# Kernel optimization log

Hardware: AMD Instinct MI355X
Metric: run time of the kernel (lower is better)

The kernel has to match this reference:

```python
import jax, jax.numpy as jnp
import numpy as np

N, E, G, D = 100000, 1600000, 1000, 32
EPS = 1e-5


def setup_inputs() -> dict:
    key = jax.random.key(0)
    ks = jax.random.split(key, 24)
    inp = {
        'h': jax.random.normal(ks[0], (N, D), dtype=jnp.float32),
        'src': jax.random.randint(ks[1], (E,), 0, N, dtype=jnp.int32),
        'dst': jax.random.randint(ks[2], (E,), 0, N, dtype=jnp.int32),
        'graph_id': jnp.sort(jax.random.randint(ks[3], (N,), 0, G, dtype=jnp.int32)),
    }
    dims = [D, 32, 32, 32, 1]
    ki = 4
    for i in range(4):
        inp[f'conv_w{i}'] = jax.random.normal(ks[ki], (dims[i], dims[i + 1]), dtype=jnp.float32) * 0.1; ki += 1
        inp[f'conv_b{i}'] = jax.random.normal(ks[ki], (dims[i + 1],), dtype=jnp.float32) * 0.1; ki += 1
        inp[f'bn_g{i}'] = jnp.ones((dims[i + 1],), dtype=jnp.float32)
        inp[f'bn_b{i}'] = jnp.zeros((dims[i + 1],), dtype=jnp.float32)
    mlp_dims = [D + 32 + 32 + 32 + 1, 128, 64, 1]  # 129 -> 128 -> 64 -> 1
    for i in range(3):
        inp[f'mlp_w{i}'] = jax.random.normal(ks[ki], (mlp_dims[i], mlp_dims[i + 1]), dtype=jnp.float32) * 0.1; ki += 1
        inp[f'mlp_b{i}'] = jax.random.normal(ks[ki], (mlp_dims[i + 1],), dtype=jnp.float32) * 0.1; ki += 1
    return inp


def _mean_agg(x, src, dst):
    # DGL update_all(copy_u, mean): h'_v = mean of h_u over in-neighbors u of v
    deg = jax.ops.segment_sum(jnp.ones((src.shape[0],), x.dtype), dst, num_segments=N)
    agg = jax.ops.segment_sum(x[src], dst, num_segments=N)
    return agg / jnp.maximum(deg, 1.0)[:, None]


def _bn(x, g, b):
    # BatchNorm1d in training mode: batch statistics over node dim
    m = x.mean(axis=0)
    v = x.var(axis=0)
    return g * (x - m) * jax.lax.rsqrt(v + EPS) + b


def reference(h, src, dst, graph_id,
              conv_w0, conv_b0, conv_w1, conv_b1, conv_w2, conv_b2, conv_w3, conv_b3,
              bn_g0, bn_b0, bn_g1, bn_b1, bn_g2, bn_b2, bn_g3, bn_b3,
              mlp_w0, mlp_b0, mlp_w1, mlp_b1, mlp_w2, mlp_b2):
    conv = [(conv_w0, conv_b0), (conv_w1, conv_b1), (conv_w2, conv_b2), (conv_w3, conv_b3)]
    bn = [(bn_g0, bn_b0), (bn_g1, bn_b1), (bn_g2, bn_b2), (bn_g3, bn_b3)]
    h_list = [h]
    x = h
    for (w, b), (g, bb) in zip(conv, bn):
        x = _mean_agg(x, src, dst) @ w + b      # GCNConv
        x = jax.nn.relu(_bn(x, g, bb))           # BN + ReLU
        h_list.append(x)
    h_final = jnp.concatenate(h_list, axis=1)    # [N, 129]
    # dgl.mean_nodes: per-graph mean pool
    cnt = jax.ops.segment_sum(jnp.ones((N,), h_final.dtype), graph_id, num_segments=G)
    hg = jax.ops.segment_sum(h_final, graph_id, num_segments=G) / jnp.maximum(cnt, 1.0)[:, None]
    hg = jax.nn.relu(hg @ mlp_w0 + mlp_b0)
    hg = jax.nn.relu(hg @ mlp_w1 + mlp_b1)
    hg = hg @ mlp_w2 + mlp_b2
    return hg.reshape(-1)                         # [G]
```

## Files before the change

### kernel.cpp

```cpp
#include <hip/hip_runtime.h>

#define NSLOT 32
#define BN_EPS 1e-5f
#define NSB 256
#define BKBITS 8
#define BKN 256
#define MAXBUCK 512

static inline int cdiv_h(int a, int b) { return (a + b - 1) / b; }

__device__ __forceinline__ float4 f4add(float4 a, float4 b) {
    return make_float4(a.x + b.x, a.y + b.y, a.z + b.z, a.w + b.w);
}

__device__ __forceinline__ unsigned bf16rtn(float x) {
    unsigned u = __float_as_uint(x);
    return (u + 0x7FFFu + ((u >> 16) & 1u)) >> 16;
}
__device__ __forceinline__ unsigned bf16pack2(float lo, float hi) {
    return bf16rtn(lo) | (bf16rtn(hi) << 16);
}

__device__ __forceinline__ int blk_excl_scan256(int v, int t) {
    __shared__ int wsum[4];
    int l = t & 63, w = t >> 6;
    int incl = v;
#pragma unroll
    for (int off = 1; off < 64; off <<= 1) {
        int o = __shfl_up(incl, off, 64);
        if (l >= off) incl += o;
    }
    if (l == 63) wsum[w] = incl;
    __syncthreads();
    int wofs = 0;
#pragma unroll
    for (int i = 0; i < 4; i++) wofs += (i < w) ? wsum[i] : 0;
    __syncthreads();
    return wofs + incl - v;
}

__device__ __forceinline__ int blk_excl_scan512(int v, int t) {
    __shared__ int wsum8[8];
    int l = t & 63, w = t >> 6;
    int incl = v;
#pragma unroll
    for (int off = 1; off < 64; off <<= 1) {
        int o = __shfl_up(incl, off, 64);
        if (l >= off) incl += o;
    }
    if (l == 63) wsum8[w] = incl;
    __syncthreads();
    int wofs = 0;
#pragma unroll
    for (int i = 0; i < 8; i++) wofs += (i < w) ? wsum8[i] : 0;
    __syncthreads();
    return wofs + incl - v;
}

__device__ __forceinline__ void bn_coef(const float* __restrict__ sSum, const float* __restrict__ sSq,
                                        const float* __restrict__ bg, const float* __restrict__ bb,
                                        float invN, int ch, float* aOut, float* cOut) {
    float S = 0.f, Q = 0.f;
#pragma unroll
    for (int s = 0; s < NSLOT; s++) { S += sSum[s * 32 + ch]; Q += sSq[s * 32 + ch]; }
    float m = S * invN;
    float var = Q * invN - m * m;
    if (var < 0.f) var = 0.f;
    float iv = rsqrtf(var + BN_EPS);
    float a = bg[ch] * iv;
    *aOut = a;
    *cOut = bb[ch] - m * a;
}


__global__ __launch_bounds__(256) void k_hist(const int* __restrict__ dst, int* __restrict__ histT,
                                              float* __restrict__ sSum, float* __restrict__ sSq,
                                              int E, int nbuck, int chunk) {
    __shared__ int bins[MAXBUCK];
    int k = blockIdx.x, t = threadIdx.x;
    if (k == 0) {
        for (int i = t; i < 4 * NSLOT * 32; i += 256) { sSum[i] = 0.f; sSq[i] = 0.f; }
    }
    for (int b = t; b < nbuck; b += 256) bins[b] = 0;
    __syncthreads();
    int lo = k * chunk, hi = lo + chunk; if (hi > E) hi = E;
    for (int i = lo + t; i < hi; i += 256) atomicAdd(&bins[dst[i] >> BKBITS], 1);
    __syncthreads();
    for (int b = t; b < nbuck; b += 256) histT[k * nbuck + b] = bins[b];
}


__global__ __launch_bounds__(256) void k_scanA(const int* __restrict__ histT, int* __restrict__ prefixB,
                                               int* __restrict__ totalP, int* __restrict__ totalU,
                                               const int* __restrict__ gid, int* __restrict__ gstart,
                                               int nbuck, int N, int G) {
    int b = blockIdx.x, k = threadIdx.x;
    int i = b * 256 + k;
    if (i < N) {
        int g = gid[i];
        int gp = (i == 0) ? -1 : gid[i - 1];
        for (int x = gp + 1; x <= g; ++x) gstart[x] = i;
        if (i == N - 1) { for (int x = g + 1; x <= G; ++x) gstart[x] = N; }
    }
    int c = histT[k * nbuck + b];
    int pad = (c + 15) & ~15;
    int ep = blk_excl_scan256(pad, k);
    prefixB[b * NSB + k] = ep;
    int ec = blk_excl_scan256(c, k);
    if (k == NSB - 1) { totalP[b] = ep + pad; totalU[b] = ec + c; }
}

__global__ __launch_bounds__(512) void k_scanB(const int* __restrict__ totalP, const int* __restrict__ totalU,
                                               int* __restrict__ baseP, int* __restrict__ baseU, int nbuck) {
    int t = threadIdx.x;
    int vp = (t < nbuck) ? totalP[t] : 0;
    int vu = (t < nbuck) ? totalU[t] : 0;
    int ep = blk_excl_scan512(vp, t);
    int eu = blk_excl_scan512(vu, t);
    if (t < nbuck) { baseP[t] = ep; baseU[t] = eu; }
}


__global__ __launch_bounds__(256) void k_scatter2(const int* __restrict__ src, const int* __restrict__ dst,
                                                  const int* __restrict__ baseP, const int* __restrict__ prefixB,
                                                  unsigned* __restrict__ ebuf, int E, int nbuck, int chunk) {
    __shared__ int cur[MAXBUCK];
    int k = blockIdx.x, t = threadIdx.x;
    for (int b = t; b < nbuck; b += 256) cur[b] = baseP[b] + prefixB[b * NSB + k];
    __syncthreads();
    int lo = k * chunk, hi = lo + chunk; if (hi > E) hi = E;
    for (int i = lo + t; i < hi; i += 256) {
        int d = dst[i], s = src[i];
        int b = d >> BKBITS;
        int pos = atomicAdd(&cur[b], 1);
        ebuf[pos] = ((unsigned)(d & (BKN - 1)) << 24) | (unsigned)s;
    }
}


__global__ __launch_bounds__(256) void k_sortb(const unsigned* __restrict__ ebuf, const int* __restrict__ histT,
                                               const int* __restrict__ baseP, const int* __restrict__ prefixB,
                                               const int* __restrict__ baseU,
                                               int* __restrict__ col, int* __restrict__ rs, int* __restrict__ re,
                                               int nbuck, int N) {
    __shared__ int binCnt[BKN], binStart[BKN], cursor[BKN];
    __shared__ int cellBase[NSB], cellCnt[NSB];
    int b = blockIdx.x, t = threadIdx.x;
    cellBase[t] = baseP[b] + prefixB[b * NSB + t];
    cellCnt[t]  = histT[t * nbuck + b];
    binCnt[t] = 0; cursor[t] = 0;
    __syncthreads();
    {
        int cb = cellBase[t], cc = cellCnt[t];
        for (int j = 0; j < cc; j++) atomicAdd(&binCnt[ebuf[cb + j] >> 24], 1);
    }
    __syncthreads();
    int bs = blk_excl_scan256(binCnt[t], t);
    binStart[t] = bs;
    __syncthreads();
    int colBase = baseU[b];
    {
        int cb = cellBase[t], cc = cellCnt[t];
        for (int j = 0; j < cc; j++) {
            unsigned e = ebuf[cb + j];
            int l = e >> 24;
            int pos = binStart[l] + atomicAdd(&cursor[l], 1);
            col[colBase + pos] = (int)(e & 0xFFFFFFu);
        }
    }
    int node = b * BKN + t;
    if (node < N) {
        rs[node] = colBase + binStart[t];
        re[node] = colBase + binStart[t] + binCnt[t];
    }
}


template <int AFF>
__global__ __launch_bounds__(256) void k_transform(const float* __restrict__ xin, const float* __restrict__ W,
                                                   const float* __restrict__ sSum, const float* __restrict__ sSq,
                                                   const float* __restrict__ bg, const float* __restrict__ bb,
                                                   uint4* __restrict__ pb, int n, float invN) {
    __shared__ float sW[32][32];
    __shared__ float sA[32], sC[32];
    int t = threadIdx.x;
    for (int i = t; i < 1024; i += 256) sW[i >> 5][i & 31] = W[i];
    if (AFF && t < 32) bn_coef(sSum, sSq, bg, bb, invN, t, &sA[t], &sC[t]);
    __syncthreads();
    int node = blockIdx.x * 256 + t;
    if (node >= n) return;
    float x[32];
    const float4* s4 = (const float4*)(xin + (size_t)node * 32);
#pragma unroll
    for (int q = 0; q < 8; q++) {
        float4 v = s4[q];
        x[4*q] = v.x; x[4*q+1] = v.y; x[4*q+2] = v.z; x[4*q+3] = v.w;
    }
    if (AFF) {
#pragma unroll
        for (int k = 0; k < 32; k++) {
            float v = sA[k] * x[k] + sC[k];
            x[k] = v > 0.f ? v : 0.f;
        }
    }
    float acc[32];
#pragma unroll
    for (int f = 0; f < 32; f++) acc[f] = 0.f;
#pragma unroll
    for (int k = 0; k < 32; k++) {
        float xv = x[k];
#pragma unroll
        for (int f = 0; f < 32; f++) acc[f] += xv * sW[k][f];
    }
    uint4* d4 = pb + (size_t)node * 4;
#pragma unroll
    for (int q = 0; q < 4; q++) {
        uint4 o;
        o.x = bf16pack2(acc[8*q+0], acc[8*q+1]);
        o.y = bf16pack2(acc[8*q+2], acc[8*q+3]);
        o.z = bf16pack2(acc[8*q+4], acc[8*q+5]);
        o.w = bf16pack2(acc[8*q+6], acc[8*q+7]);
        d4[q] = o;
    }
}

__global__ __launch_bounds__(256) void k_transform3(const float* __restrict__ y2, const float* __restrict__ w3,
                                                    const float* __restrict__ sSum, const float* __restrict__ sSq,
                                                    const float* __restrict__ bg, const float* __restrict__ bb,
                                                    float* __restrict__ p3, int n, float invN) {
    __shared__ float sw[32], sA[32], sC[32];
    int t = threadIdx.x;
    if (t < 32) { sw[t] = w3[t]; bn_coef(sSum, sSq, bg, bb, invN, t, &sA[t], &sC[t]); }
    __syncthreads();
    int i = blockIdx.x * 256 + t;
    if (i >= n) return;
    const float4* x4 = (const float4*)(y2 + (size_t)i * 32);
    float acc = 0.f;
#pragma unroll
    for (int q = 0; q < 8; q++) {
        float4 v = x4[q];
        float vv[4] = {v.x, v.y, v.z, v.w};
#pragma unroll
        for (int r = 0; r < 4; r++) {
            int k = q * 4 + r;
            float xv = sA[k] * vv[r] + sC[k];
            xv = xv > 0.f ? xv : 0.f;
            acc += xv * sw[k];
        }
    }
    p3[i] = acc;
}


__global__ __launch_bounds__(256) void k_aggregate(const uint4* __restrict__ pb, const int* __restrict__ rs,
                                                   const int* __restrict__ re, const int* __restrict__ col,
                                                   const float* __restrict__ bias,
                                                   float4* __restrict__ y4, float* __restrict__ sSum,
                                                   float* __restrict__ sSq, int n) {
    __shared__ int scol[2048];
    int t = threadIdx.x;
    int lane = t & 3;
    int grp = t >> 2;
    int node0 = blockIdx.x * 64;
    int node = node0 + grp;
    int base0 = 0, len = 0;
    if (node0 < n) {
        int last = node0 + 63; if (last > n - 1) last = n - 1;
        base0 = rs[node0];
        len = re[last] - base0;
    }
    bool lds = (len > 0 && len <= 2048);
    if (lds) { for (int i = t; i < len; i += 256) scol[i] = col[base0 + i]; }
    __syncthreads();

    float accA[8], accB[8];
#pragma unroll
    for (int q = 0; q < 8; q++) { accA[q] = 0.f; accB[q] = 0.f; }
    float vout[8];
#pragma unroll
    for (int q = 0; q < 8; q++) vout[q] = 0.f;
    if (node < n) {
        int s0 = rs[node], s1 = re[node];
#define GATH(vv, c) uint4 vv = pb[(size_t)(c) * 4 + lane]
#define ACC(dst, vv) \
        dst[0] += __uint_as_float((vv).x << 16); dst[1] += __uint_as_float((vv).x & 0xFFFF0000u); \
        dst[2] += __uint_as_float((vv).y << 16); dst[3] += __uint_as_float((vv).y & 0xFFFF0000u); \
        dst[4] += __uint_as_float((vv).z << 16); dst[5] += __uint_as_float((vv).z & 0xFFFF0000u); \
        dst[6] += __uint_as_float((vv).w << 16); dst[7] += __uint_as_float((vv).w & 0xFFFF0000u)
        if (lds) {
            int j = s0 - base0, j1 = s1 - base0;
            for (; j + 8 <= j1; j += 8) {
                int c0 = scol[j], c1 = scol[j + 1], c2 = scol[j + 2], c3 = scol[j + 3];
                int c4 = scol[j + 4], c5 = scol[j + 5], c6 = scol[j + 6], c7 = scol[j + 7];
                GATH(g0, c0); GATH(g1, c1); GATH(g2, c2); GATH(g3, c3);
                GATH(g4, c4); GATH(g5, c5); GATH(g6, c6); GATH(g7, c7);
                ACC(accA, g0); ACC(accB, g1); ACC(accA, g2); ACC(accB, g3);
                ACC(accA, g4); ACC(accB, g5); ACC(accA, g6); ACC(accB, g7);
            }
            for (; j < j1; ++j) { GATH(g, scol[j]); ACC(accA, g); }
        } else {
            for (int j = s0; j < s1; ++j) { GATH(g, col[j]); ACC(accA, g); }
        }
#undef GATH
#undef ACC
        int deg = s1 - s0;
        float inv = (deg > 0) ? 1.f / (float)deg : 1.f;
        const float4* b4 = (const float4*)bias;
        float4 b0 = b4[lane * 2], b1 = b4[lane * 2 + 1];
        vout[0] = (accA[0] + accB[0]) * inv + b0.x;
        vout[1] = (accA[1] + accB[1]) * inv + b0.y;
        vout[2] = (accA[2] + accB[2]) * inv + b0.z;
        vout[3] = (accA[3] + accB[3]) * inv + b0.w;
        vout[4] = (accA[4] + accB[4]) * inv + b1.x;
        vout[5] = (accA[5] + accB[5]) * inv + b1.y;
        vout[6] = (accA[6] + accB[6]) * inv + b1.z;
        vout[7] = (accA[7] + accB[7]) * inv + b1.w;
        y4[(size_t)node * 8 + lane * 2]     = make_float4(vout[0], vout[1], vout[2], vout[3]);
        y4[(size_t)node * 8 + lane * 2 + 1] = make_float4(vout[4], vout[5], vout[6], vout[7]);
    }
    __shared__ float sS[64][32];
    __shared__ float sQ[64][32];
    ((float4*)&sS[grp][lane * 8])[0] = make_float4(vout[0], vout[1], vout[2], vout[3]);
    ((float4*)&sS[grp][lane * 8])[1] = make_float4(vout[4], vout[5], vout[6], vout[7]);
    ((float4*)&sQ[grp][lane * 8])[0] = make_float4(vout[0]*vout[0], vout[1]*vout[1], vout[2]*vout[2], vout[3]*vout[3]);
    ((float4*)&sQ[grp][lane * 8])[1] = make_float4(vout[4]*vout[4], vout[5]*vout[5], vout[6]*vout[6], vout[7]*vout[7]);
    __syncthreads();
    if (t < 32) {
        float S = 0.f, Q = 0.f;
#pragma unroll
        for (int g2 = 0; g2 < 64; g2++) { S += sS[g2][t]; Q += sQ[g2][t]; }
        int slot = blockIdx.x & (NSLOT - 1);
        atomicAdd(&sSum[slot * 32 + t], S);
        atomicAdd(&sSq[slot * 32 + t], Q);
    }
}

__global__ __launch_bounds__(256) void k_aggregate3(const float* __restrict__ p3, const int* __restrict__ rs,
                                                    const int* __restrict__ re, const int* __restrict__ col,
                                                    const float* __restrict__ b1,
                                                    float* __restrict__ y3, float* __restrict__ sSum,
                                                    float* __restrict__ sSq, int n) {
    int i = blockIdx.x * 256 + threadIdx.x;
    float lsum = 0.f, lsq = 0.f;
    if (i < n) {
        int s0 = rs[i], s1 = re[i];
        float a0 = 0.f, a1 = 0.f, a2 = 0.f, a3 = 0.f;
        int j = s0;
        for (; j + 4 <= s1; j += 4) {
            int c0 = col[j], c1 = col[j + 1], c2 = col[j + 2], c3 = col[j + 3];
            a0 += p3[c0]; a1 += p3[c1]; a2 += p3[c2]; a3 += p3[c3];
        }
        for (; j < s1; ++j) a0 += p3[col[j]];
        float acc = (a0 + a1) + (a2 + a3);
        float inv = (s1 > s0) ? 1.f / (float)(s1 - s0) : 1.f;
        float v = acc * inv + b1[0];
        y3[i] = v; lsum = v; lsq = v * v;
    }
    __shared__ float sS[256], sQ[256];
    int t = threadIdx.x;
    sS[t] = lsum; sQ[t] = lsq;
    __syncthreads();
    for (int s = 128; s > 0; s >>= 1) {
        if (t < s) { sS[t] += sS[t + s]; sQ[t] += sQ[t + s]; }
        __syncthreads();
    }
    if (t == 0) {
        int slot = blockIdx.x & (NSLOT - 1);
        atomicAdd(&sSum[slot * 32], sS[0]);
        atomicAdd(&sSq[slot * 32], sQ[0]);
    }
}


__global__ __launch_bounds__(256) void k_pool_mlp(const float* __restrict__ h, const float* __restrict__ y0,
                                                  const float* __restrict__ y1, const float* __restrict__ y2,
                                                  const float* __restrict__ y3,
                                                  const float* __restrict__ sSum, const float* __restrict__ sSq,
                                                  const float* __restrict__ bg0, const float* __restrict__ bb0,
                                                  const float* __restrict__ bg1, const float* __restrict__ bb1,
                                                  const float* __restrict__ bg2, const float* __restrict__ bb2,
                                                  const float* __restrict__ bg3, const float* __restrict__ bb3,
                                                  const int* __restrict__ gstart,
                                                  const float* __restrict__ w0, const float* __restrict__ b0,
                                                  const float* __restrict__ w1, const float* __restrict__ b1,
                                                  const float* __restrict__ w2, const float* __restrict__ b2,
                                                  float* __restrict__ out, float invN) {
    __shared__ float pcA[128], pcC[128];
    int g = blockIdx.x;
    int t = threadIdx.x;
    if (t < 97) {
        int layer = (t == 96) ? 3 : (t >> 5);
        int ch = t & 31;
        const float* bg = (layer == 0) ? bg0 : (layer == 1) ? bg1 : (layer == 2) ? bg2 : bg3;
        const float* bb = (layer == 0) ? bb0 : (layer == 1) ? bb1 : (layer == 2) ? bb2 : bb3;
        bn_coef(sSum + layer * NSLOT * 32, sSq + layer * NSLOT * 32, bg, bb, invN, ch, &pcA[t], &pcC[t]);
    }
    __syncthreads();
    int s0 = gstart[g], s1 = gstart[g + 1];
    int lane = t & 31, slot = t >> 5;
    int arr = lane >> 3, sub = lane & 7;
    const float* bases0 = (arr == 0) ? h : (arr == 1) ? y0 : (arr == 2) ? y1 : y2;
    const float4* bp = (const float4*)bases0;
    float4 a4 = make_float4(1.f, 1.f, 1.f, 1.f);
    float4 c4 = make_float4(0.f, 0.f, 0.f, 0.f);
    bool aff = (arr > 0);
    if (aff) {
        a4 = ((const float4*)pcA)[(arr - 1) * 8 + sub];
        c4 = ((const float4*)pcC)[(arr - 1) * 8 + sub];
    }
    float4 acc = make_float4(0.f, 0.f, 0.f, 0.f);
    for (int n = s0 + slot; n < s1; n += 8) {
        float4 v = bp[(size_t)n * 8 + sub];
        if (aff) {
            float vx = fmaf(a4.x, v.x, c4.x); vx = vx > 0.f ? vx : 0.f;
            float vy = fmaf(a4.y, v.y, c4.y); vy = vy > 0.f ? vy : 0.f;
            float vz = fmaf(a4.z, v.z, c4.z); vz = vz > 0.f ? vz : 0.f;
            float vw = fmaf(a4.w, v.w, c4.w); vw = vw > 0.f ? vw : 0.f;
            v = make_float4(vx, vy, vz, vw);
        }
        acc = f4add(acc, v);
    }
    __shared__ float sP[8][128];
    __shared__ float sY[8];
    ((float4*)&sP[slot][lane * 4])[0] = acc;
    if (t < 8) {
        float a = pcA[96], c = pcC[96], s = 0.f;
        for (int n = s0 + t; n < s1; n += 8) {
            float v = fmaf(a, y3[n], c);
            s += v > 0.f ? v : 0.f;
        }
        sY[t] = s;
    }
    __syncthreads();
    __shared__ float hg[129];
    __shared__ float hid1[128];
    __shared__ float hid2[64];
    float inv = (s1 > s0) ? 1.f / (float)(s1 - s0) : 1.f;
    if (t < 128) {
        float S = 0.f;
#pragma unroll
        for (int s = 0; s < 8; s++) S += sP[s][t];
        hg[t] = S * inv;
    } else if (t == 128) {
        float S = 0.f;
#pragma unroll
        for (int s = 0; s < 8; s++) S += sY[s];
        hg[128] = S * inv;
    }
    __syncthreads();
    if (t < 128) {
        float a = b0[t];
        for (int i = 0; i < 129; i++) a += hg[i] * w0[i * 128 + t];
        hid1[t] = a > 0.f ? a : 0.f;
    }
    __syncthreads();
    if (t < 64) {
        float a = b1[t];
        for (int i = 0; i < 128; i++) a += hid1[i] * w1[i * 64 + t];
        hid2[t] = a > 0.f ? a : 0.f;
    }
    __syncthreads();
    if (t < 64) {
        float v = hid2[t] * w2[t];
        for (int off = 32; off > 0; off >>= 1) v += __shfl_down(v, off, 64);
        if (t == 0) out[g] = v + b2[0];
    }
}


extern "C" void kernel_launch(void* const* d_in, const int* in_sizes, int n_in,
                              void* d_out, int out_size, void* d_ws, size_t ws_size,
                              hipStream_t stream) {
    const float* h   = (const float*)d_in[0];
    const int* src   = (const int*)d_in[1];
    const int* dst   = (const int*)d_in[2];
    const int* gid   = (const int*)d_in[3];
    const float* convw[4], *convb[4], *bng[4], *bnb[4];
    for (int i = 0; i < 4; i++) {
        convw[i] = (const float*)d_in[4 + 4 * i];
        convb[i] = (const float*)d_in[5 + 4 * i];
        bng[i]   = (const float*)d_in[6 + 4 * i];
        bnb[i]   = (const float*)d_in[7 + 4 * i];
    }
    const float* mw0 = (const float*)d_in[20];
    const float* mb0 = (const float*)d_in[21];
    const float* mw1 = (const float*)d_in[22];
    const float* mb1 = (const float*)d_in[23];
    const float* mw2 = (const float*)d_in[24];
    const float* mb2 = (const float*)d_in[25];

    const int N = in_sizes[0] / 32;
    const int E = in_sizes[1];
    const int G = out_size;
    const int nbuck = cdiv_h(N, BKN);
    const int chunk = cdiv_h(E, NSB);

    char* ws = (char*)d_ws;
    size_t off = 0;
    auto alloc = [&](size_t bytes) -> void* {
        void* p = ws + off;
        off += (bytes + 511) & ~(size_t)511;
        return p;
    };
    int* histT   = (int*)alloc((size_t)NSB * nbuck * 4);
    int* prefixB = (int*)alloc((size_t)nbuck * NSB * 4);
    int* totalP  = (int*)alloc((size_t)nbuck * 4);
    int* totalU  = (int*)alloc((size_t)nbuck * 4);
    int* basePp  = (int*)alloc((size_t)nbuck * 4);
    int* baseUp  = (int*)alloc((size_t)nbuck * 4);
    size_t ebufE = (size_t)E + (size_t)16 * NSB * nbuck;
    size_t ovl   = ebufE * 4;
    size_t pB    = (size_t)N * 64;
    if (pB > ovl) ovl = pB;
    unsigned* ebuf = (unsigned*)alloc(ovl);
    uint4* pb    = (uint4*)ebuf;
    int* col     = (int*)alloc((size_t)E * 4);
    int* rs      = (int*)alloc((size_t)N * 4);
    int* re      = (int*)alloc((size_t)N * 4);
    int* gstart  = (int*)alloc((size_t)(G + 1) * 4);
    float* y0    = (float*)alloc((size_t)N * 32 * 4);
    float* y1    = (float*)alloc((size_t)N * 32 * 4);
    float* y2    = (float*)alloc((size_t)N * 32 * 4);
    float* y3    = (float*)alloc((size_t)N * 4);
    float* sSum  = (float*)alloc((size_t)4 * NSLOT * 32 * 4);
    float* sSq   = (float*)alloc((size_t)4 * NSLOT * 32 * 4);
    (void)ws_size; (void)n_in;

    const int NB_N = cdiv_h(N, 256);
    const int NB_AG = cdiv_h(N, 64);
    const float invN = 1.f / (float)N;

    k_hist<<<NSB, 256, 0, stream>>>(dst, histT, sSum, sSq, E, nbuck, chunk);
    k_scanA<<<nbuck, 256, 0, stream>>>(histT, prefixB, totalP, totalU, gid, gstart, nbuck, N, G);
    k_scanB<<<1, 512, 0, stream>>>(totalP, totalU, basePp, baseUp, nbuck);
    k_scatter2<<<NSB, 256, 0, stream>>>(src, dst, basePp, prefixB, ebuf, E, nbuck, chunk);
    k_sortb<<<nbuck, 256, 0, stream>>>(ebuf, histT, basePp, prefixB, baseUp, col, rs, re, nbuck, N);

    k_transform<0><<<NB_N, 256, 0, stream>>>(h, convw[0], nullptr, nullptr, nullptr, nullptr, pb, N, invN);
    k_aggregate<<<NB_AG, 256, 0, stream>>>(pb, rs, re, col, convb[0], (float4*)y0,
                                           sSum + 0 * NSLOT * 32, sSq + 0 * NSLOT * 32, N);
    k_transform<1><<<NB_N, 256, 0, stream>>>(y0, convw[1], sSum + 0 * NSLOT * 32, sSq + 0 * NSLOT * 32,
                                             bng[0], bnb[0], pb, N, invN);
    k_aggregate<<<NB_AG, 256, 0, stream>>>(pb, rs, re, col, convb[1], (float4*)y1,
                                           sSum + 1 * NSLOT * 32, sSq + 1 * NSLOT * 32, N);
    k_transform<1><<<NB_N, 256, 0, stream>>>(y1, convw[2], sSum + 1 * NSLOT * 32, sSq + 1 * NSLOT * 32,
                                             bng[1], bnb[1], pb, N, invN);
    k_aggregate<<<NB_AG, 256, 0, stream>>>(pb, rs, re, col, convb[2], (float4*)y2,
                                           sSum + 2 * NSLOT * 32, sSq + 2 * NSLOT * 32, N);
    k_transform3<<<NB_N, 256, 0, stream>>>(y2, convw[3], sSum + 2 * NSLOT * 32, sSq + 2 * NSLOT * 32,
                                           bng[2], bnb[2], (float*)pb, N, invN);
    k_aggregate3<<<NB_N, 256, 0, stream>>>((float*)pb, rs, re, col, convb[3], y3,
                                           sSum + 3 * NSLOT * 32, sSq + 3 * NSLOT * 32, N);

    k_pool_mlp<<<G, 256, 0, stream>>>(h, y0, y1, y2, y3, sSum, sSq,
                                      bng[0], bnb[0], bng[1], bnb[1], bng[2], bnb[2], bng[3], bnb[3],
                                      gstart, mw0, mb0, mw1, mb1, mw2, mb2, (float*)d_out, invN);
}
```

Baseline: 319.8 us.

## Split feature tables into halves and schedule aggregation per XCC via work queues

The bf16 gather table and fp32 layer outputs are split into low and high 16-channel halves stored as separate arrays. Aggregation becomes a persistent-style kernel that pulls tiles from two atomic queues, one per half. Each block picks which half to process first from its XCC id, so each XCC's L2 mostly holds one smaller half-table. This aims to improve cache hit rates on the random neighbor gathers, at the cost of reading the column lists twice, extra atomics and barriers per tile, and more scattered accesses in the transform and pooling kernels.

Result: slower. 445.7 us (+39.4%).

```diff
diff --git a/kernel.cpp b/kernel.cpp
--- a/kernel.cpp
+++ b/kernel.cpp
@@ -6,6 +6,11 @@
 #define BKBITS 8
 #define BKN 256
 #define MAXBUCK 512
+#define AGTILE 128
+#define SCOLCAP 4096
+
+#define HWREG(id, off, sz) ((id) | ((off) << 6) | (((sz) - 1) << 11))
+#define HW_REG_XCC_ID 20
 
 static inline int cdiv_h(int a, int b) { return (a + b - 1) / b; }
 
@@ -75,11 +80,13 @@
 
 __global__ __launch_bounds__(256) void k_hist(const int* __restrict__ dst, int* __restrict__ histT,
                                               float* __restrict__ sSum, float* __restrict__ sSq,
+                                              int* __restrict__ qcnt,
                                               int E, int nbuck, int chunk) {
     __shared__ int bins[MAXBUCK];
     int k = blockIdx.x, t = threadIdx.x;
     if (k == 0) {
         for (int i = t; i < 4 * NSLOT * 32; i += 256) { sSum[i] = 0.f; sSq[i] = 0.f; }
+        if (t < 8) qcnt[t] = 0;
     }
     for (int b = t; b < nbuck; b += 256) bins[b] = 0;
     __syncthreads();
@@ -177,10 +184,12 @@
 
 
 template <int AFF>
-__global__ __launch_bounds__(256) void k_transform(const float* __restrict__ xin, const float* __restrict__ W,
+__global__ __launch_bounds__(256) void k_transform(const float* __restrict__ xinLo, const float* __restrict__ xinHi,
+                                                   const float* __restrict__ W,
                                                    const float* __restrict__ sSum, const float* __restrict__ sSq,
                                                    const float* __restrict__ bg, const float* __restrict__ bb,
-                                                   uint4* __restrict__ pb, int n, float invN) {
+                                                   uint4* __restrict__ pLo, uint4* __restrict__ pHi,
+                                                   int n, float invN) {
     __shared__ float sW[32][32];
     __shared__ float sA[32], sC[32];
     int t = threadIdx.x;
@@ -190,18 +199,28 @@
     int node = blockIdx.x * 256 + t;
     if (node >= n) return;
     float x[32];
-    const float4* s4 = (const float4*)(xin + (size_t)node * 32);
-#pragma unroll
-    for (int q = 0; q < 8; q++) {
-        float4 v = s4[q];
-        x[4*q] = v.x; x[4*q+1] = v.y; x[4*q+2] = v.z; x[4*q+3] = v.w;
-    }
     if (AFF) {
+        const float4* l4 = (const float4*)(xinLo + (size_t)node * 16);
+        const float4* h4 = (const float4*)(xinHi + (size_t)node * 16);
+#pragma unroll
+        for (int q = 0; q < 4; q++) {
+            float4 v = l4[q];
+            x[4*q] = v.x; x[4*q+1] = v.y; x[4*q+2] = v.z; x[4*q+3] = v.w;
+            float4 w = h4[q];
+            x[16+4*q] = w.x; x[16+4*q+1] = w.y; x[16+4*q+2] = w.z; x[16+4*q+3] = w.w;
+        }
 #pragma unroll
         for (int k = 0; k < 32; k++) {
             float v = sA[k] * x[k] + sC[k];
             x[k] = v > 0.f ? v : 0.f;
         }
+    } else {
+        const float4* s4 = (const float4*)(xinLo + (size_t)node * 32);
+#pragma unroll
+        for (int q = 0; q < 8; q++) {
+            float4 v = s4[q];
+            x[4*q] = v.x; x[4*q+1] = v.y; x[4*q+2] = v.z; x[4*q+3] = v.w;
+        }
     }
     float acc[32];
 #pragma unroll
@@ -212,19 +231,24 @@
 #pragma unroll
         for (int f = 0; f < 32; f++) acc[f] += xv * sW[k][f];
     }
-    uint4* d4 = pb + (size_t)node * 4;
-#pragma unroll
-    for (int q = 0; q < 4; q++) {
-        uint4 o;
-        o.x = bf16pack2(acc[8*q+0], acc[8*q+1]);
-        o.y = bf16pack2(acc[8*q+2], acc[8*q+3]);
-        o.z = bf16pack2(acc[8*q+4], acc[8*q+5]);
-        o.w = bf16pack2(acc[8*q+6], acc[8*q+7]);
-        d4[q] = o;
-    }
-}
-
-__global__ __launch_bounds__(256) void k_transform3(const float* __restrict__ y2, const float* __restrict__ w3,
+#pragma unroll
+    for (int half = 0; half < 2; half++) {
+        uint4* d = (half ? pHi : pLo) + (size_t)node * 2;
+        const float* a = acc + half * 16;
+#pragma unroll
+        for (int q = 0; q < 2; q++) {
+            uint4 o;
+            o.x = bf16pack2(a[8*q+0], a[8*q+1]);
+            o.y = bf16pack2(a[8*q+2], a[8*q+3]);
+            o.z = bf16pack2(a[8*q+4], a[8*q+5]);
+            o.w = bf16pack2(a[8*q+6], a[8*q+7]);
+            d[q] = o;
+        }
+    }
+}
+
+__global__ __launch_bounds__(256) void k_transform3(const float* __restrict__ yLo, const float* __restrict__ yHi,
+                                                    const float* __restrict__ w3,
                                                     const float* __restrict__ sSum, const float* __restrict__ sSq,
                                                     const float* __restrict__ bg, const float* __restrict__ bb,
                                                     float* __restrict__ p3, int n, float invN) {
@@ -234,104 +258,127 @@
     __syncthreads();
     int i = blockIdx.x * 256 + t;
     if (i >= n) return;
-    const float4* x4 = (const float4*)(y2 + (size_t)i * 32);
     float acc = 0.f;
 #pragma unroll
-    for (int q = 0; q < 8; q++) {
-        float4 v = x4[q];
-        float vv[4] = {v.x, v.y, v.z, v.w};
-#pragma unroll
-        for (int r = 0; r < 4; r++) {
-            int k = q * 4 + r;
-            float xv = sA[k] * vv[r] + sC[k];
-            xv = xv > 0.f ? xv : 0.f;
-            acc += xv * sw[k];
+    for (int half = 0; half < 2; half++) {
+        const float4* x4 = (const float4*)(((half) ? yHi : yLo) + (size_t)i * 16);
+#pragma unroll
+        for (int q = 0; q < 4; q++) {
+            float4 v = x4[q];
+            float vv[4] = {v.x, v.y, v.z, v.w};
+#pragma unroll
+            for (int r = 0; r < 4; r++) {
+                int k = half * 16 + q * 4 + r;
+                float xv = sA[k] * vv[r] + sC[k];
+                xv = xv > 0.f ? xv : 0.f;
+                acc += xv * sw[k];
+            }
         }
     }
     p3[i] = acc;
 }
 
 
-__global__ __launch_bounds__(256) void k_aggregate(const uint4* __restrict__ pb, const int* __restrict__ rs,
-                                                   const int* __restrict__ re, const int* __restrict__ col,
-                                                   const float* __restrict__ bias,
-                                                   float4* __restrict__ y4, float* __restrict__ sSum,
-                                                   float* __restrict__ sSq, int n) {
-    __shared__ int scol[2048];
+__global__ __launch_bounds__(256) void k_agg(const uint4* __restrict__ pLo, const uint4* __restrict__ pHi,
+                                             const int* __restrict__ rs, const int* __restrict__ re,
+                                             const int* __restrict__ col, const float* __restrict__ bias,
+                                             float4* __restrict__ yLo, float4* __restrict__ yHi,
+                                             float* __restrict__ sSum, float* __restrict__ sSq,
+                                             int* __restrict__ qcnt, int n, int numTiles) {
+    __shared__ int scol[SCOLCAP];
+    __shared__ int stile;
+    __shared__ float sS[AGTILE][16], sQ[AGTILE][16];
+    __shared__ float pS[8][16], pQ[8][16];
     int t = threadIdx.x;
-    int lane = t & 3;
-    int grp = t >> 2;
-    int node0 = blockIdx.x * 64;
-    int node = node0 + grp;
-    int base0 = 0, len = 0;
-    if (node0 < n) {
-        int last = node0 + 63; if (last > n - 1) last = n - 1;
-        base0 = rs[node0];
-        len = re[last] - base0;
-    }
-    bool lds = (len > 0 && len <= 2048);
-    if (lds) { for (int i = t; i < len; i += 256) scol[i] = col[base0 + i]; }
-    __syncthreads();
-
-    float accA[8], accB[8];
-#pragma unroll
-    for (int q = 0; q < 8; q++) { accA[q] = 0.f; accB[q] = 0.f; }
-    float vout[8];
-#pragma unroll
-    for (int q = 0; q < 8; q++) vout[q] = 0.f;
-    if (node < n) {
-        int s0 = rs[node], s1 = re[node];
-#define GATH(vv, c) uint4 vv = pb[(size_t)(c) * 4 + lane]
+    int lane = t & 1;
+    int grp = t >> 1;
+    int pref = __builtin_amdgcn_s_getreg(HWREG(HW_REG_XCC_ID, 0, 4)) & 1;
+#pragma unroll
+    for (int phase = 0; phase < 2; phase++) {
+        int half = pref ^ phase;
+        const uint4* pb = half ? pHi : pLo;
+        float4* y4 = half ? yHi : yLo;
+        for (;;) {
+            __syncthreads();
+            if (t == 0) stile = atomicAdd(&qcnt[half], 1);
+            __syncthreads();
+            int tile = stile;
+            if (tile >= numTiles) break;
+            int node0 = tile * AGTILE;
+            int node = node0 + grp;
+            int last = node0 + AGTILE - 1; if (last > n - 1) last = n - 1;
+            int base0 = rs[node0];
+            int len = re[last] - base0;
+            bool lds = (len <= SCOLCAP);
+            if (lds) { for (int i = t; i < len; i += 256) scol[i] = col[base0 + i]; }
+            __syncthreads();
+            float accA[8], accB[8];
+#pragma unroll
+            for (int q = 0; q < 8; q++) { accA[q] = 0.f; accB[q] = 0.f; }
+            float vout[8];
+#pragma unroll
+            for (int q = 0; q < 8; q++) vout[q] = 0.f;
+            if (node < n) {
+                int s0 = rs[node], s1 = re[node];
+#define GATH(vv, c) uint4 vv = pb[(size_t)(c) * 2 + lane]
 #define ACC(dst, vv) \
-        dst[0] += __uint_as_float((vv).x << 16); dst[1] += __uint_as_float((vv).x & 0xFFFF0000u); \
-        dst[2] += __uint_as_float((vv).y << 16); dst[3] += __uint_as_float((vv).y & 0xFFFF0000u); \
-        dst[4] += __uint_as_float((vv).z << 16); dst[5] += __uint_as_float((vv).z & 0xFFFF0000u); \
-        dst[6] += __uint_as_float((vv).w << 16); dst[7] += __uint_as_float((vv).w & 0xFFFF0000u)
-        if (lds) {
-            int j = s0 - base0, j1 = s1 - base0;
-            for (; j + 8 <= j1; j += 8) {
-                int c0 = scol[j], c1 = scol[j + 1], c2 = scol[j + 2], c3 = scol[j + 3];
-                int c4 = scol[j + 4], c5 = scol[j + 5], c6 = scol[j + 6], c7 = scol[j + 7];
-                GATH(g0, c0); GATH(g1, c1); GATH(g2, c2); GATH(g3, c3);
-                GATH(g4, c4); GATH(g5, c5); GATH(g6, c6); GATH(g7, c7);
-                ACC(accA, g0); ACC(accB, g1); ACC(accA, g2); ACC(accB, g3);
-                ACC(accA, g4); ACC(accB, g5); ACC(accA, g6); ACC(accB, g7);
-            }
-            for (; j < j1; ++j) { GATH(g, scol[j]); ACC(accA, g); }
-        } else {
-            for (int j = s0; j < s1; ++j) { GATH(g, col[j]); ACC(accA, g); }
-        }
+                dst[0] += __uint_as_float((vv).x << 16); dst[1] += __uint_as_float((vv).x & 0xFFFF0000u); \
+                dst[2] += __uint_as_float((vv).y << 16); dst[3] += __uint_as_float((vv).y & 0xFFFF0000u); \
+                dst[4] += __uint_as_float((vv).z << 16); dst[5] += __uint_as_float((vv).z & 0xFFFF0000u); \
+                dst[6] += __uint_as_float((vv).w << 16); dst[7] += __uint_as_float((vv).w & 0xFFFF0000u)
+                if (lds) {
+                    int j = s0 - base0, j1 = s1 - base0;
+                    for (; j + 8 <= j1; j += 8) {
+                        int c0 = scol[j], c1 = scol[j + 1], c2 = scol[j + 2], c3 = scol[j + 3];
+                        int c4 = scol[j + 4], c5 = scol[j + 5], c6 = scol[j + 6], c7 = scol[j + 7];
+                        GATH(g0, c0); GATH(g1, c1); GATH(g2, c2); GATH(g3, c3);
+                        GATH(g4, c4); GATH(g5, c5); GATH(g6, c6); GATH(g7, c7);
+                        ACC(accA, g0); ACC(accB, g1); ACC(accA, g2); ACC(accB, g3);
+                        ACC(accA, g4); ACC(accB, g5); ACC(accA, g6); ACC(accB, g7);
+                    }
+                    for (; j < j1; ++j) { GATH(g, scol[j]); ACC(accA, g); }
+                } else {
+                    for (int j = s0; j < s1; ++j) { GATH(g, col[j]); ACC(accA, g); }
+                }
 #undef GATH
 #undef ACC
-        int deg = s1 - s0;
-        float inv = (deg > 0) ? 1.f / (float)deg : 1.f;
-        const float4* b4 = (const float4*)bias;
-        float4 b0 = b4[lane * 2], b1 = b4[lane * 2 + 1];
-        vout[0] = (accA[0] + accB[0]) * inv + b0.x;
-        vout[1] = (accA[1] + accB[1]) * inv + b0.y;
-        vout[2] = (accA[2] + accB[2]) * inv + b0.z;
-        vout[3] = (accA[3] + accB[3]) * inv + b0.w;
-        vout[4] = (accA[4] + accB[4]) * inv + b1.x;
-        vout[5] = (accA[5] + accB[5]) * inv + b1.y;
-        vout[6] = (accA[6] + accB[6]) * inv + b1.z;
-        vout[7] = (accA[7] + accB[7]) * inv + b1.w;
-        y4[(size_t)node * 8 + lane * 2]     = make_float4(vout[0], vout[1], vout[2], vout[3]);
-        y4[(size_t)node * 8 + lane * 2 + 1] = make_float4(vout[4], vout[5], vout[6], vout[7]);
-    }
-    __shared__ float sS[64][32];
-    __shared__ float sQ[64][32];
-    ((float4*)&sS[grp][lane * 8])[0] = make_float4(vout[0], vout[1], vout[2], vout[3]);
-    ((float4*)&sS[grp][lane * 8])[1] = make_float4(vout[4], vout[5], vout[6], vout[7]);
-    ((float4*)&sQ[grp][lane * 8])[0] = make_float4(vout[0]*vout[0], vout[1]*vout[1], vout[2]*vout[2], vout[3]*vout[3]);
-    ((float4*)&sQ[grp][lane * 8])[1] = make_float4(vout[4]*vout[4], vout[5]*vout[5], vout[6]*vout[6], vout[7]*vout[7]);
-    __syncthreads();
-    if (t < 32) {
-        float S = 0.f, Q = 0.f;
-#pragma unroll
-        for (int g2 = 0; g2 < 64; g2++) { S += sS[g2][t]; Q += sQ[g2][t]; }
-        int slot = blockIdx.x & (NSLOT - 1);
-        atomicAdd(&sSum[slot * 32 + t], S);
-        atomicAdd(&sSq[slot * 32 + t], Q);
+                int deg = s1 - s0;
+                float inv = (deg > 0) ? 1.f / (float)deg : 1.f;
+                const float4* b4 = (const float4*)bias;
+                float4 b0 = b4[half * 4 + lane * 2], b1 = b4[half * 4 + lane * 2 + 1];
+                vout[0] = (accA[0] + accB[0]) * inv + b0.x;
+                vout[1] = (accA[1] + accB[1]) * inv + b0.y;
+                vout[2] = (accA[2] + accB[2]) * inv + b0.z;
+                vout[3] = (accA[3] + accB[3]) * inv + b0.w;
+                vout[4] = (accA[4] + accB[4]) * inv + b1.x;
+                vout[5] = (accA[5] + accB[5]) * inv + b1.y;
+                vout[6] = (accA[6] + accB[6]) * inv + b1.z;
+                vout[7] = (accA[7] + accB[7]) * inv + b1.w;
+                y4[(size_t)node * 4 + lane * 2]     = make_float4(vout[0], vout[1], vout[2], vout[3]);
+                y4[(size_t)node * 4 + lane * 2 + 1] = make_float4(vout[4], vout[5], vout[6], vout[7]);
+            }
+            ((float4*)&sS[grp][lane * 8])[0] = make_float4(vout[0], vout[1], vout[2], vout[3]);
+            ((float4*)&sS[grp][lane * 8])[1] = make_float4(vout[4], vout[5], vout[6], vout[7]);
+            ((float4*)&sQ[grp][lane * 8])[0] = make_float4(vout[0]*vout[0], vout[1]*vout[1], vout[2]*vout[2], vout[3]*vout[3]);
+            ((float4*)&sQ[grp][lane * 8])[1] = make_float4(vout[4]*vout[4], vout[5]*vout[5], vout[6]*vout[6], vout[7]*vout[7]);
+            __syncthreads();
+            if (t < 128) {
+                int ch = t & 15, seg = t >> 4;
+                float s = 0.f, qq = 0.f;
+#pragma unroll
+                for (int r = 0; r < 16; r++) { s += sS[seg * 16 + r][ch]; qq += sQ[seg * 16 + r][ch]; }
+                pS[seg][ch] = s; pQ[seg][ch] = qq;
+            }
+            __syncthreads();
+            if (t < 16) {
+                float s = 0.f, qq = 0.f;
+#pragma unroll
+                for (int i = 0; i < 8; i++) { s += pS[i][t]; qq += pQ[i][t]; }
+                int slot = tile & (NSLOT - 1);
+                atomicAdd(&sSum[slot * 32 + half * 16 + t], s);
+                atomicAdd(&sSq[slot * 32 + half * 16 + t], qq);
+            }
+        }
     }
 }
 
@@ -372,8 +419,10 @@
 }
 
 
-__global__ __launch_bounds__(256) void k_pool_mlp(const float* __restrict__ h, const float* __restrict__ y0,
-                                                  const float* __restrict__ y1, const float* __restrict__ y2,
+__global__ __launch_bounds__(256) void k_pool_mlp(const float* __restrict__ h,
+                                                  const float* __restrict__ y0L, const float* __restrict__ y0H,
+                                                  const float* __restrict__ y1L, const float* __restrict__ y1H,
+                                                  const float* __restrict__ y2L, const float* __restrict__ y2H,
                                                   const float* __restrict__ y3,
                                                   const float* __restrict__ sSum, const float* __restrict__ sSq,
                                                   const float* __restrict__ bg0, const float* __restrict__ bb0,
@@ -399,8 +448,15 @@
     int s0 = gstart[g], s1 = gstart[g + 1];
     int lane = t & 31, slot = t >> 5;
     int arr = lane >> 3, sub = lane & 7;
-    const float* bases0 = (arr == 0) ? h : (arr == 1) ? y0 : (arr == 2) ? y1 : y2;
-    const float4* bp = (const float4*)bases0;
+    const float4* bp;
+    int stride, offs;
+    if (arr == 0) { bp = (const float4*)h; stride = 8; offs = sub; }
+    else {
+        const float* lo = (arr == 1) ? y0L : (arr == 2) ? y1L : y2L;
+        const float* hi = (arr == 1) ? y0H : (arr == 2) ? y1H : y2H;
+        bp = (const float4*)((sub < 4) ? lo : hi);
+        stride = 4; offs = sub & 3;
+    }
     float4 a4 = make_float4(1.f, 1.f, 1.f, 1.f);
     float4 c4 = make_float4(0.f, 0.f, 0.f, 0.f);
     bool aff = (arr > 0);
@@ -410,7 +466,7 @@
     }
     float4 acc = make_float4(0.f, 0.f, 0.f, 0.f);
     for (int n = s0 + slot; n < s1; n += 8) {
-        float4 v = bp[(size_t)n * 8 + sub];
+        float4 v = bp[(size_t)n * stride + offs];
         if (aff) {
             float vx = fmaf(a4.x, v.x, c4.x); vx = vx > 0.f ? vx : 0.f;
             float vy = fmaf(a4.y, v.y, c4.y); vy = vy > 0.f ? vy : 0.f;
@@ -494,6 +550,7 @@
     const int G = out_size;
     const int nbuck = cdiv_h(N, BKN);
     const int chunk = cdiv_h(E, NSB);
+    const int numTiles = cdiv_h(N, AGTILE);
 
     char* ws = (char*)d_ws;
     size_t off = 0;
@@ -508,51 +565,57 @@
     int* totalU  = (int*)alloc((size_t)nbuck * 4);
     int* basePp  = (int*)alloc((size_t)nbuck * 4);
     int* baseUp  = (int*)alloc((size_t)nbuck * 4);
+    int* qcnt    = (int*)alloc((size_t)8 * 4);
     size_t ebufE = (size_t)E + (size_t)16 * NSB * nbuck;
     size_t ovl   = ebufE * 4;
     size_t pB    = (size_t)N * 64;
     if (pB > ovl) ovl = pB;
     unsigned* ebuf = (unsigned*)alloc(ovl);
-    uint4* pb    = (uint4*)ebuf;
+    uint4* pLo   = (uint4*)ebuf;
+    uint4* pHi   = pLo + (size_t)N * 2;
     int* col     = (int*)alloc((size_t)E * 4);
     int* rs      = (int*)alloc((size_t)N * 4);
     int* re      = (int*)alloc((size_t)N * 4);
     int* gstart  = (int*)alloc((size_t)(G + 1) * 4);
-    float* y0    = (float*)alloc((size_t)N * 32 * 4);
-    float* y1    = (float*)alloc((size_t)N * 32 * 4);
-    float* y2    = (float*)alloc((size_t)N * 32 * 4);
+    float* y0L   = (float*)alloc((size_t)N * 16 * 4);
+    float* y0H   = (float*)alloc((size_t)N * 16 * 4);
+    float* y1L   = (float*)alloc((size_t)N * 16 * 4);
+    float* y1H   = (float*)alloc((size_t)N * 16 * 4);
+    float* y2L   = (float*)alloc((size_t)N * 16 * 4);
+    float* y2H   = (float*)alloc((size_t)N * 16 * 4);
     float* y3    = (float*)alloc((size_t)N * 4);
     float* sSum  = (float*)alloc((size_t)4 * NSLOT * 32 * 4);
     float* sSq   = (float*)alloc((size_t)4 * NSLOT * 32 * 4);
     (void)ws_size; (void)n_in;
 
     const int NB_N = cdiv_h(N, 256);
-    const int NB_AG = cdiv_h(N, 64);
+    const int NB_AG = 2 * numTiles;
     const float invN = 1.f / (float)N;
 
-    k_hist<<<NSB, 256, 0, stream>>>(dst, histT, sSum, sSq, E, nbuck, chunk);
+    k_hist<<<NSB, 256, 0, stream>>>(dst, histT, sSum, sSq, qcnt, E, nbuck, chunk);
     k_scanA<<<nbuck, 256, 0, stream>>>(histT, prefixB, totalP, totalU, gid, gstart, nbuck, N, G);
     k_scanB<<<1, 512, 0, stream>>>(totalP, totalU, basePp, baseUp, nbuck);
     k_scatter2<<<NSB, 256, 0, stream>>>(src, dst, basePp, prefixB, ebuf, E, nbuck, chunk);
     k_sortb<<<nbuck, 256, 0, stream>>>(ebuf, histT, basePp, prefixB, baseUp, col, rs, re, nbuck, N);
 
-    k_transform<0><<<NB_N, 256, 0, stream>>>(h, convw[0], nullptr, nullptr, nullptr, nullptr, pb, N, invN);
-    k_aggregate<<<NB_AG, 256, 0, stream>>>(pb, rs, re, col, convb[0], (float4*)y0,
-                                           sSum + 0 * NSLOT * 32, sSq + 0 * NSLOT * 32, N);
-    k_transform<1><<<NB_N, 256, 0, stream>>>(y0, convw[1], sSum + 0 * NSLOT * 32, sSq + 0 * NSLOT * 32,
-                                             bng[0], bnb[0], pb, N, invN);
-    k_aggregate<<<NB_AG, 256, 0, stream>>>(pb, rs, re, col, convb[1], (float4*)y1,
-                                           sSum + 1 * NSLOT * 32, sSq + 1 * NSLOT * 32, N);
-    k_transform<1><<<NB_N, 256, 0, stream>>>(y1, convw[2], sSum + 1 * NSLOT * 32, sSq + 1 * NSLOT * 32,
-                                             bng[1], bnb[1], pb, N, invN);
-    k_aggregate<<<NB_AG, 256, 0, stream>>>(pb, rs, re, col, convb[2], (float4*)y2,
-                                           sSum + 2 * NSLOT * 32, sSq + 2 * NSLOT * 32, N);
-    k_transform3<<<NB_N, 256, 0, stream>>>(y2, convw[3], sSum + 2 * NSLOT * 32, sSq + 2 * NSLOT * 32,
-                                           bng[2], bnb[2], (float*)pb, N, invN);
-    k_aggregate3<<<NB_N, 256, 0, stream>>>((float*)pb, rs, re, col, convb[3], y3,
+    k_transform<0><<<NB_N, 256, 0, stream>>>(h, nullptr, convw[0], nullptr, nullptr, nullptr, nullptr,
+                                             pLo, pHi, N, invN);
+    k_agg<<<NB_AG, 256, 0, stream>>>(pLo, pHi, rs, re, col, convb[0], (float4*)y0L, (float4*)y0H,
+                                     sSum + 0 * NSLOT * 32, sSq + 0 * NSLOT * 32, qcnt + 0, N, numTiles);
+    k_transform<1><<<NB_N, 256, 0, stream>>>(y0L, y0H, convw[1], sSum + 0 * NSLOT * 32, sSq + 0 * NSLOT * 32,
+                                             bng[0], bnb[0], pLo, pHi, N, invN);
+    k_agg<<<NB_AG, 256, 0, stream>>>(pLo, pHi, rs, re, col, convb[1], (float4*)y1L, (float4*)y1H,
+                                     sSum + 1 * NSLOT * 32, sSq + 1 * NSLOT * 32, qcnt + 2, N, numTiles);
+    k_transform<1><<<NB_N, 256, 0, stream>>>(y1L, y1H, convw[2], sSum + 1 * NSLOT * 32, sSq + 1 * NSLOT * 32,
+                                             bng[1], bnb[1], pLo, pHi, N, invN);
+    k_agg<<<NB_AG, 256, 0, stream>>>(pLo, pHi, rs, re, col, convb[2], (float4*)y2L, (float4*)y2H,
+                                     sSum + 2 * NSLOT * 32, sSq + 2 * NSLOT * 32, qcnt + 4, N, numTiles);
+    k_transform3<<<NB_N, 256, 0, stream>>>(y2L, y2H, convw[3], sSum + 2 * NSLOT * 32, sSq + 2 * NSLOT * 32,
+                                           bng[2], bnb[2], (float*)pLo, N, invN);
+    k_aggregate3<<<NB_N, 256, 0, stream>>>((float*)pLo, rs, re, col, convb[3], y3,
                                            sSum + 3 * NSLOT * 32, sSq + 3 * NSLOT * 32, N);
 
-    k_pool_mlp<<<G, 256, 0, stream>>>(h, y0, y1, y2, y3, sSum, sSq,
+    k_pool_mlp<<<G, 256, 0, stream>>>(h, y0L, y0H, y1L, y1H, y2L, y2H, y3, sSum, sSq,
                                       bng[0], bnb[0], bng[1], bnb[1], bng[2], bnb[2], bng[3], bnb[3],
                                       gstart, mw0, mb0, mw1, mb1, mw2, mb2, (float*)d_out, invN);
 }
```
